# Optimization experiments

Measured on AMD Instinct MI355X. Metric: run time of the kernel, lower is better.

Reference implementation:

```python
import jax, jax.numpy as jnp
import numpy as np

N = 300000   # total nodes
C = 32       # hidden states
M = 64       # discrete label alphabet
NGEN = 8     # number of generative models
G = 8192     # number of graphs


def setup_inputs() -> dict:
    key = jax.random.key(0)
    k1, k2, k3, k4 = jax.random.split(key, 4)
    B = jax.random.uniform(k1, (C, M, NGEN), minval=-5.0, maxval=5.0, dtype=jnp.float32)
    Pi = jax.random.uniform(k2, (C, NGEN), minval=-5.0, maxval=5.0, dtype=jnp.float32)
    x = jax.random.randint(k3, (N,), 0, M)
    batch = jnp.sort(jax.random.randint(k4, (N,), 0, G))
    return {"B": B, "Pi": Pi, "x": x, "batch": batch, "num_graphs": G}


def reference(B, Pi, x, batch, num_graphs):
    # softmax reparameterization: over M for B, over C for Pi (per generator)
    sm_B = jax.nn.softmax(B, axis=1)          # (C, M, n_gen)
    sm_Pi = jax.nn.softmax(Pi, axis=0)        # (C, n_gen)
    # gather per-node emission probs, then joint with prior -> (N, C, n_gen)
    numerator = sm_Pi[None, :, :] * jnp.transpose(sm_B[:, x, :], (1, 0, 2))
    posterior = numerator / numerator.sum(axis=1, keepdims=True)  # (N, C, n_gen)
    likelihood = (posterior * jnp.log(numerator)).sum(axis=1)     # (N, n_gen)
    # scatter-sum per graph
    likelihood = jax.ops.segment_sum(likelihood, batch, num_segments=num_graphs)  # (G, n_gen)
    h_vals = posterior.max(axis=1, keepdims=True)   # (N, 1, n_gen)
    h_idx = posterior.argmax(axis=1)                # (N, n_gen)
    return likelihood, h_vals, h_idx
```

## Files before the change

kernel.cpp:

```cpp
#include <hip/hip_runtime.h>

#define C_DIM 32
#define M_DIM 64
#define NG    8
#define TAB   (M_DIM * NG)
#define ST    9
#define BST   520
#define SPB   1024
#define NTB   8


__global__ void __launch_bounds__(256)
cgmm_prep(const float* __restrict__ B, const float* __restrict__ Pi,
          const int* __restrict__ batch,
          float* __restrict__ tab, int* __restrict__ starts,
          int N, int G) {
    const int tid = threadIdx.x;
    const int bid = blockIdx.x;

    if (bid < NTB) {
        __shared__ float Bs[C_DIM * BST];
        __shared__ float Pis[C_DIM * NG];
        __shared__ float lsePi_s[NG];
        __shared__ float K_s[C_DIM * NG];

        const float4* B4 = (const float4*)B;
        float4* Bs4 = (float4*)Bs;
        #pragma unroll
        for (int i = tid; i < (C_DIM * M_DIM * NG) / 4; i += 256)
            Bs4[(i >> 7) * (BST / 4) + (i & 127)] = B4[i];
        if (tid < C_DIM * NG / 4) ((float4*)Pis)[tid] = ((const float4*)Pi)[tid];
        __syncthreads();

        if (tid < NG) {
            float s = 0.f;
            #pragma unroll
            for (int c = 0; c < C_DIM; ++c) s += __expf(Pis[c * NG + tid]);
            lsePi_s[tid] = __logf(s);
        }
        __syncthreads();

        {
            const int g = tid & 7;
            const float* bp = Bs + (tid >> 3) * BST + g;
            float s = 0.f;
            #pragma unroll
            for (int m = 0; m < M_DIM; ++m) s += __expf(bp[m * NG]);
            K_s[tid] = Pis[tid] - __logf(s) - lsePi_s[g];
        }
        __syncthreads();

        if (tid < 64) {
            const int m = bid * NTB + (tid >> 3);
            const int g = tid & 7;
            float L[C_DIM];
            float best = -1e30f; int bidx = 0;
            #pragma unroll
            for (int c = 0; c < C_DIM; ++c) {
                float v = Bs[c * BST + m * NG + g] + K_s[c * NG + g];
                L[c] = v;
                if (v > best) { best = v; bidx = c; }
            }
            float se = 0.f, la = 0.f;
            #pragma unroll
            for (int c = 0; c < C_DIM; ++c) {
                float e = __expf(L[c] - best);
                se += e; la += e * L[c];
            }
            const int idx = m * NG + g;
            tab[idx]           = la / se;
            tab[TAB + idx]     = 1.f / se;
            tab[2 * TAB + idx] = (float)bidx;
        }
        return;
    }

    const int base = (bid - NTB) * SPB;
    for (int i = tid; i < SPB; i += 256) {
        const int n = base + i;
        if (n >= N) break;
        const int bn = batch[n];
        if (n == 0) {
            for (int j = 0; j <= bn; ++j) starts[j] = 0;
        } else {
            const int bp = batch[n - 1];
            for (int j = bp + 1; j <= bn; ++j) starts[j] = n;
        }
        if (n == N - 1) {
            for (int j = bn + 1; j <= G; ++j) starts[j] = N;
        }
    }
}

__global__ void __launch_bounds__(512)
cgmm_write(const int* __restrict__ x, const int* __restrict__ starts,
           const float* __restrict__ tab,
           float* __restrict__ out_like, float* __restrict__ out_hv,
           float* __restrict__ out_hi, int G) {
    __shared__ float like_s[M_DIM * ST];
    __shared__ float hval_s[M_DIM * ST];
    __shared__ float hidx_s[M_DIM * ST];
    const int tid = threadIdx.x;
    for (int i = tid; i < TAB; i += 512) {
        const int p = (i >> 3) * ST + (i & 7);
        like_s[p] = tab[i];
        hval_s[p] = tab[TAB + i];
        hidx_s[p] = tab[2 * TAB + i];
    }
    __syncthreads();

    const int j = blockIdx.x * 8 + (tid >> 6);
    if (j >= G) return;
    const int start = starts[j];
    const int end   = starts[j + 1];

    const int lane = tid & 63;
    const int slot = lane >> 3;
    const int g    = lane & 7;

    float4* hv4 = (float4*)out_hv;
    float4* hi4 = (float4*)out_hi;

    float acc = 0.f;
    for (int cb = start; cb < end; cb += 64) {
        const int cnt = end - cb;
        const int xv  = (cb + lane < end) ? x[cb + lane] : 0;

        #pragma unroll
        for (int s = 0; s < 2; ++s) {
            const int f    = s * 64 + lane;
            const int node = f >> 1;
            const int h    = (f & 1) * 4;
            const int xm   = __shfl(xv, node);
            if (node < cnt) {
                const int p = xm * ST + h;
                float4 v, w;
                v.x = hval_s[p];     v.y = hval_s[p + 1];
                v.z = hval_s[p + 2]; v.w = hval_s[p + 3];
                w.x = hidx_s[p];     w.y = hidx_s[p + 1];
                w.z = hidx_s[p + 2]; w.w = hidx_s[p + 3];
                hv4[(size_t)cb * 2 + f] = v;
                hi4[(size_t)cb * 2 + f] = w;
            }
        }
        #pragma unroll
        for (int t = 0; t < 8; ++t) {
            const int node = slot + 8 * t;
            const int xm   = __shfl(xv, node);
            if (node < cnt) acc += like_s[xm * ST + g];
        }
    }
    acc += __shfl_xor(acc, 8);
    acc += __shfl_xor(acc, 16);
    acc += __shfl_xor(acc, 32);
    if (lane < NG) out_like[(size_t)j * NG + g] = acc;
}

extern "C" void kernel_launch(void* const* d_in, const int* in_sizes, int n_in,
                              void* d_out, int out_size, void* d_ws, size_t ws_size,
                              hipStream_t stream) {
    const float* B     = (const float*)d_in[0];
    const float* Pi    = (const float*)d_in[1];
    const int*   x     = (const int*)d_in[2];
    const int*   batch = (const int*)d_in[3];
    const int N = in_sizes[2];
    const int G = (out_size - 2 * N * NG) / NG;

    float* tab    = (float*)d_ws;
    int*   starts = (int*)((char*)d_ws + 16384);

    float* out_like = (float*)d_out;
    float* out_hv   = out_like + (size_t)G * NG;
    float* out_hi   = out_hv + (size_t)N * NG;

    const int nsb = (N + SPB - 1) / SPB;

    cgmm_prep<<<NTB + nsb, 256, 0, stream>>>(B, Pi, batch, tab, starts, N, G);
    cgmm_write<<<(G + 7) / 8, 512, 0, stream>>>(x, starts, tab, out_like,
                                                out_hv, out_hi, G);
}
```

Before: 17.99 us.

## Replace segment-start scan with per-block binary search over sorted batch

The prep kernel no longer scans all of batch to build a starts array. It now launches only the 8 table-building blocks. Each write block instead binary-searches the sorted batch array for its 9 segment boundaries and keeps them in shared memory. This drops a full pass over batch plus the starts write and reread, at the cost of about 19 dependent global loads per boundary thread before the block can proceed.

```diff
diff --git a/kernel.cpp b/kernel.cpp
--- a/kernel.cpp
+++ b/kernel.cpp
@@ -6,113 +6,103 @@
 #define TAB   (M_DIM * NG)
 #define ST    9
 #define BST   520
-#define SPB   1024
 #define NTB   8
 
 
 __global__ void __launch_bounds__(256)
-cgmm_prep(const float* __restrict__ B, const float* __restrict__ Pi,
-          const int* __restrict__ batch,
-          float* __restrict__ tab, int* __restrict__ starts,
-          int N, int G) {
+cgmm_tables(const float* __restrict__ B, const float* __restrict__ Pi,
+            float* __restrict__ tab) {
+    __shared__ float Bs[C_DIM * BST];
+    __shared__ float Pis[C_DIM * NG];
+    __shared__ float lsePi_s[NG];
+    __shared__ float K_s[C_DIM * NG];
+
     const int tid = threadIdx.x;
     const int bid = blockIdx.x;
 
-    if (bid < NTB) {
-        __shared__ float Bs[C_DIM * BST];
-        __shared__ float Pis[C_DIM * NG];
-        __shared__ float lsePi_s[NG];
-        __shared__ float K_s[C_DIM * NG];
+    const float4* B4 = (const float4*)B;
+    float4* Bs4 = (float4*)Bs;
+    #pragma unroll
+    for (int i = tid; i < (C_DIM * M_DIM * NG) / 4; i += 256)
+        Bs4[(i >> 7) * (BST / 4) + (i & 127)] = B4[i];
+    if (tid < C_DIM * NG / 4) ((float4*)Pis)[tid] = ((const float4*)Pi)[tid];
+    __syncthreads();
 
-        const float4* B4 = (const float4*)B;
-        float4* Bs4 = (float4*)Bs;
+    if (tid < NG) {
+        float s = 0.f;
         #pragma unroll
-        for (int i = tid; i < (C_DIM * M_DIM * NG) / 4; i += 256)
-            Bs4[(i >> 7) * (BST / 4) + (i & 127)] = B4[i];
-        if (tid < C_DIM * NG / 4) ((float4*)Pis)[tid] = ((const float4*)Pi)[tid];
-        __syncthreads();
+        for (int c = 0; c < C_DIM; ++c) s += __expf(Pis[c * NG + tid]);
+        lsePi_s[tid] = __logf(s);
+    }
+    __syncthreads();
 
-        if (tid < NG) {
-            float s = 0.f;
-            #pragma unroll
-            for (int c = 0; c < C_DIM; ++c) s += __expf(Pis[c * NG + tid]);
-            lsePi_s[tid] = __logf(s);
+    {
+        const int g = tid & 7;
+        const float* bp = Bs + (tid >> 3) * BST + g;
+        float s = 0.f;
+        #pragma unroll
+        for (int m = 0; m < M_DIM; ++m) s += __expf(bp[m * NG]);
+        K_s[tid] = Pis[tid] - __logf(s) - lsePi_s[g];
+    }
+    __syncthreads();
+
+    if (tid < 64) {
+        const int m = bid * NTB + (tid >> 3);
+        const int g = tid & 7;
+        float L[C_DIM];
+        float best = -1e30f; int bidx = 0;
+        #pragma unroll
+        for (int c = 0; c < C_DIM; ++c) {
+            float v = Bs[c * BST + m * NG + g] + K_s[c * NG + g];
+            L[c] = v;
+            if (v > best) { best = v; bidx = c; }
         }
-        __syncthreads();
-
-        {
-            const int g = tid & 7;
-            const float* bp = Bs + (tid >> 3) * BST + g;
-            float s = 0.f;
-            #pragma unroll
-            for (int m = 0; m < M_DIM; ++m) s += __expf(bp[m * NG]);
-            K_s[tid] = Pis[tid] - __logf(s) - lsePi_s[g];
+        float se = 0.f, la = 0.f;
+        #pragma unroll
+        for (int c = 0; c < C_DIM; ++c) {
+            float e = __expf(L[c] - best);
+            se += e; la += e * L[c];
         }
-        __syncthreads();
-
-        if (tid < 64) {
-            const int m = bid * NTB + (tid >> 3);
-            const int g = tid & 7;
-            float L[C_DIM];
-            float best = -1e30f; int bidx = 0;
-            #pragma unroll
-            for (int c = 0; c < C_DIM; ++c) {
-                float v = Bs[c * BST + m * NG + g] + K_s[c * NG + g];
-                L[c] = v;
-                if (v > best) { best = v; bidx = c; }
-            }
-            float se = 0.f, la = 0.f;
-            #pragma unroll
-            for (int c = 0; c < C_DIM; ++c) {
-                float e = __expf(L[c] - best);
-                se += e; la += e * L[c];
-            }
-            const int idx = m * NG + g;
-            tab[idx]           = la / se;
-            tab[TAB + idx]     = 1.f / se;
-            tab[2 * TAB + idx] = (float)bidx;
-        }
-        return;
-    }
-
-    const int base = (bid - NTB) * SPB;
-    for (int i = tid; i < SPB; i += 256) {
-        const int n = base + i;
-        if (n >= N) break;
-        const int bn = batch[n];
-        if (n == 0) {
-            for (int j = 0; j <= bn; ++j) starts[j] = 0;
-        } else {
-            const int bp = batch[n - 1];
-            for (int j = bp + 1; j <= bn; ++j) starts[j] = n;
-        }
-        if (n == N - 1) {
-            for (int j = bn + 1; j <= G; ++j) starts[j] = N;
-        }
+        const int idx = m * NG + g;
+        tab[idx]           = la / se;
+        tab[TAB + idx]     = 1.f / se;
+        tab[2 * TAB + idx] = (float)bidx;
     }
 }
 
 __global__ void __launch_bounds__(512)
-cgmm_write(const int* __restrict__ x, const int* __restrict__ starts,
+cgmm_write(const int* __restrict__ x, const int* __restrict__ batch,
            const float* __restrict__ tab,
            float* __restrict__ out_like, float* __restrict__ out_hv,
-           float* __restrict__ out_hi, int G) {
+           float* __restrict__ out_hi, int N, int G) {
     __shared__ float like_s[M_DIM * ST];
     __shared__ float hval_s[M_DIM * ST];
     __shared__ float hidx_s[M_DIM * ST];
+    __shared__ int   bound[9];
     const int tid = threadIdx.x;
+
     for (int i = tid; i < TAB; i += 512) {
         const int p = (i >> 3) * ST + (i & 7);
         like_s[p] = tab[i];
         hval_s[p] = tab[TAB + i];
         hidx_s[p] = tab[2 * TAB + i];
     }
+    if (tid < 9) {
+        const int target = blockIdx.x * 8 + tid;
+        int lo = 0, hi = N;
+        while (lo < hi) {
+            const int mid = (lo + hi) >> 1;
+            if (batch[mid] < target) lo = mid + 1; else hi = mid;
+        }
+        bound[tid] = lo;
+    }
     __syncthreads();
 
-    const int j = blockIdx.x * 8 + (tid >> 6);
+    const int w = tid >> 6;
+    const int j = blockIdx.x * 8 + w;
     if (j >= G) return;
-    const int start = starts[j];
-    const int end   = starts[j + 1];
+    const int start = bound[w];
+    const int end   = bound[w + 1];
 
     const int lane = tid & 63;
     const int slot = lane >> 3;
@@ -134,13 +124,13 @@
             const int xm   = __shfl(xv, node);
             if (node < cnt) {
                 const int p = xm * ST + h;
-                float4 v, w;
-                v.x = hval_s[p];     v.y = hval_s[p + 1];
-                v.z = hval_s[p + 2]; v.w = hval_s[p + 3];
-                w.x = hidx_s[p];     w.y = hidx_s[p + 1];
-                w.z = hidx_s[p + 2]; w.w = hidx_s[p + 3];
+                float4 v, wv;
+                v.x  = hval_s[p];     v.y  = hval_s[p + 1];
+                v.z  = hval_s[p + 2]; v.w  = hval_s[p + 3];
+                wv.x = hidx_s[p];     wv.y = hidx_s[p + 1];
+                wv.z = hidx_s[p + 2]; wv.w = hidx_s[p + 3];
                 hv4[(size_t)cb * 2 + f] = v;
-                hi4[(size_t)cb * 2 + f] = w;
+                hi4[(size_t)cb * 2 + f] = wv;
             }
         }
         #pragma unroll
@@ -166,16 +156,13 @@
     const int N = in_sizes[2];
     const int G = (out_size - 2 * N * NG) / NG;
 
-    float* tab    = (float*)d_ws;
-    int*   starts = (int*)((char*)d_ws + 16384);
+    float* tab = (float*)d_ws;
 
     float* out_like = (float*)d_out;
     float* out_hv   = out_like + (size_t)G * NG;
     float* out_hi   = out_hv + (size_t)N * NG;
 
-    const int nsb = (N + SPB - 1) / SPB;
-
-    cgmm_prep<<<NTB + nsb, 256, 0, stream>>>(B, Pi, batch, tab, starts, N, G);
-    cgmm_write<<<(G + 7) / 8, 512, 0, stream>>>(x, starts, tab, out_like,
-                                                out_hv, out_hi, G);
+    cgmm_tables<<<NTB, 256, 0, stream>>>(B, Pi, tab);
+    cgmm_write<<<(G + 7) / 8, 512, 0, stream>>>(x, batch, tab, out_like,
+                                                out_hv, out_hi, N, G);
 }
```

Measured after the change: 21.41 us. +19.0%, slower.
